# Optimization experiments

Hardware: AMD Instinct MI355X
Metric: run time of the kernel (lower is better)

## Reference

```python
import jax, jax.numpy as jnp
import numpy as np

DIM = 1024
HEADS = 8
HD = DIM // HEADS          # 128
HALF = HD // 2             # 64 complex pairs
EPS = 1e-6
T, L, H, W = 10, 4, 21, 37
TOK_PER_FRAME = 1 + L * (5 + H * W)   # 3129
SK = T * TOK_PER_FRAME                # 31290
SQ = 512
THETA = 10000.0


def _inv_freqs(dim):
    # matches precompute_freqs_cis: 1/theta**(arange(0,dim,2)/dim)
    return 1.0 / THETA ** (np.arange(0, dim, 2)[: dim // 2].astype(np.float64) / dim)


def _angles(t_idx, h_idx, w_idx):
    # 3D RoPE split per precompute_freqs_cis_3d: f gets HD-2*(HD//3)=44 dims, h/w get HD//3=42 each
    hd3 = HD // 3
    inv_f = _inv_freqs(HD - 2 * hd3)  # 22 freqs
    inv_h = _inv_freqs(hd3)           # 21 freqs
    inv_w = _inv_freqs(hd3)           # 21 freqs
    ang = np.concatenate([
        t_idx[:, None] * inv_f[None, :],
        h_idx[:, None] * inv_h[None, :],
        w_idx[:, None] * inv_w[None, :],
    ], axis=-1)  # [S, 64]
    return ang


def _memory_positions():
    # per-frame layout from build_3d_freqs_unified: 1 pose token (h=w=0),
    # then per layer: 5 register tokens (h=w=0) + H*W grid tokens
    h_f, w_f = [0], [0]
    grid_h, grid_w = np.meshgrid(np.arange(H), np.arange(W), indexing='ij')
    for _ in range(L):
        h_f += [0] * 5 + list(grid_h.ravel())
        w_f += [0] * 5 + list(grid_w.ravel())
    h_f = np.asarray(h_f, np.float64)
    w_f = np.asarray(w_f, np.float64)
    t_idx = np.repeat(np.arange(T, dtype=np.float64), TOK_PER_FRAME)
    return t_idx, np.tile(h_f, T), np.tile(w_f, T)


def setup_inputs() -> dict:
    key = jax.random.key(0)
    ks = jax.random.split(key, 8)
    # RoPE angle tables
    tq = np.zeros(SQ)  # use_time_encoding=False for queries -> t=0
    hq = (np.arange(SQ) // W) % H
    wq = np.arange(SQ) % W
    ang_q = _angles(tq.astype(np.float64), hq.astype(np.float64), wq.astype(np.float64))
    tk, hk, wk = _memory_positions()
    ang_k = _angles(tk, hk, wk)
    s = 0.02
    inp = {
        'x': jax.random.normal(ks[0], (1, SQ, DIM), jnp.float32),
        'mem': jax.random.normal(ks[1], (1, SK, DIM), jnp.float32),
        'mask': jax.random.randint(ks[2], (1, SK), 0, 2) > 0,
        'cos_q': jnp.asarray(np.cos(ang_q), jnp.float32),
        'sin_q': jnp.asarray(np.sin(ang_q), jnp.float32),
        'cos_k': jnp.asarray(np.cos(ang_k), jnp.float32),
        'sin_k': jnp.asarray(np.sin(ang_k), jnp.float32),
        'Wq': jax.random.normal(ks[3], (DIM, DIM), jnp.float32) * s,
        'bq': jnp.zeros((DIM,), jnp.float32),
        'Wk': jax.random.normal(ks[4], (DIM, DIM), jnp.float32) * s,
        'bk': jnp.zeros((DIM,), jnp.float32),
        'Wv': jax.random.normal(ks[5], (DIM, DIM), jnp.float32) * s,
        'bv': jnp.zeros((DIM,), jnp.float32),
        'Wo': jax.random.normal(ks[6], (DIM, DIM), jnp.float32) * s,
        'bo': jnp.zeros((DIM,), jnp.float32),
        'gq': jnp.ones((DIM,), jnp.float32),
        'gk': jnp.ones((DIM,), jnp.float32),
    }
    return inp


def _rmsnorm(x, g):
    xf = x.astype(jnp.float32)
    y = xf * jax.lax.rsqrt(jnp.mean(xf * xf, axis=-1, keepdims=True) + EPS)
    return y.astype(x.dtype) * g


def _rope(x, cos, sin):
    # x: [B,S,D]; complex rotation on interleaved pairs per head, freqs shared across heads
    B, S, _ = x.shape
    xh = x.reshape(B, S, HEADS, HALF, 2)
    xr, xi = xh[..., 0], xh[..., 1]
    c = cos[None, :, None, :]
    s = sin[None, :, None, :]
    orr = xr * c - xi * s
    oi = xr * s + xi * c
    return jnp.stack([orr, oi], axis=-1).reshape(B, S, HEADS * HD)


def reference(x, mem, mask, cos_q, sin_q, cos_k, sin_k,
              Wq, bq, Wk, bk, Wv, bv, Wo, bo, gq, gk):
    q = _rmsnorm(x @ Wq.T + bq, gq)
    k = _rmsnorm(mem @ Wk.T + bk, gk)
    v = mem @ Wv.T + bv
    q = _rope(q, cos_q, sin_q)
    k = _rope(k, cos_k, sin_k)
    B, Sq, _ = q.shape
    Sk = k.shape[1]
    qh = q.reshape(B, Sq, HEADS, HD)
    kh = k.reshape(B, Sk, HEADS, HD)
    vh = v.reshape(B, Sk, HEADS, HD)
    scores = jnp.einsum('bqnd,bknd->bnqk', qh, kh) / jnp.sqrt(jnp.float32(HD))
    bias = jnp.where(mask[:, None, None, :], 0.0, -jnp.inf).astype(scores.dtype)
    attn = jax.nn.softmax(scores + bias, axis=-1)
    out = jnp.einsum('bnqk,bknd->bqnd', attn, vh).reshape(B, Sq, DIM)
    return out @ Wo.T + bo
```

## Files before the change

kernel.cpp:

```cpp
#include <hip/hip_runtime.h>
#include <cstdint>

typedef __bf16 bf16;
typedef __bf16 bf16x8 __attribute__((ext_vector_type(8)));
typedef __bf16 bf16x4 __attribute__((ext_vector_type(4)));
typedef float f32x4 __attribute__((ext_vector_type(4)));

#define DEVINL __device__ __forceinline__

namespace {
constexpr int DIM = 1024, HEADS = 8, HD = 128, HALF = 64;
constexpr int SQ = 512;
constexpr int SK = 31290;
constexpr int SKP = 31488;
constexpr int NSPLIT = 24;

constexpr long OFF_MEMB = 0;
constexpr long OFF_XB   = OFF_MEMB + (long)SKP * DIM * 2;
constexpr long OFF_WKV  = OFF_XB + (long)SQ * DIM * 2;
constexpr long OFF_WQ   = OFF_WKV + 2048L * DIM * 2;
constexpr long OFF_WO   = OFF_WQ + (long)DIM * DIM * 2;
constexpr long OFF_BKV  = OFF_WO + (long)DIM * DIM * 2;
constexpr long OFF_KPRE = OFF_BKV + 2048L * 4;
constexpr long OFF_VT   = OFF_KPRE + (long)SKP * DIM * 2;
constexpr long OFF_QPRE = OFF_VT + (long)DIM * SKP * 2;
constexpr long OFF_QR   = OFF_QPRE + (long)SQ * DIM * 4;
constexpr long OFF_ML   = OFF_QR + (long)SQ * DIM * 2;
constexpr long OFF_AO   = OFF_ML + (long)NSPLIT * HEADS * SQ * 2 * 4;
constexpr long OFF_IDX  = OFF_AO + (long)SQ * DIM * 2;
constexpr long OFF_NKC  = OFF_IDX + 31744L * 4;
constexpr long OFF_OP   = OFF_MEMB;
}

DEVINL void gl_lds16(const void* g, void* l) {
  __builtin_amdgcn_global_load_lds(
      (__attribute__((address_space(1))) void*)(void*)g,
      (__attribute__((address_space(3))) void*)l, 16, 0, 0);
}


__global__ __launch_bounds__(1024) void k_scan(const int* __restrict__ mask,
                                               int* __restrict__ idx,
                                               int* __restrict__ nkcp) {
  int tid = threadIdx.x, lane = tid & 63, wv = tid >> 6;
  __shared__ int wsum[16];
  __shared__ int base;
  if (tid == 0) base = 0;
  __syncthreads();
  for (int c = 0; c < 31; ++c) {
    int i = c * 1024 + tid;
    int m = (i < SK) ? (mask[i] != 0) : 0;
    unsigned long long bal = __ballot(m);
    int wpre = (int)__popcll(bal & ((1ull << lane) - 1ull));
    if (lane == 0) wsum[wv] = (int)__popcll(bal);
    __syncthreads();
    int woff = 0;
    #pragma unroll
    for (int j = 0; j < 16; ++j) woff += (j < wv) ? wsum[j] : 0;
    if (m) idx[base + woff + wpre] = i;
    __syncthreads();
    if (tid == 0) {
      int tot = 0;
      #pragma unroll
      for (int j = 0; j < 16; ++j) tot += wsum[j];
      base += tot;
    }
    __syncthreads();
  }
  if (tid == 0) *nkcp = base;
}


__global__ __launch_bounds__(256) void k_cvt_mem(const float* __restrict__ mem,
                                                 const int* __restrict__ idx,
                                                 const int* __restrict__ nkcp,
                                                 bf16* __restrict__ memb) {
  long i = (long)blockIdx.x * 256 + threadIdx.x;
  long e = i * 8;
  if (e >= (long)SKP * DIM) return;
  int row = (int)(e >> 10);
  int nkc = *nkcp;
  int lim = ((((nkc + 63) & ~63) + 255) & ~255);
  if (row >= lim) return;
  bf16x8 o;
  if (row < nkc) {
    long se = ((long)idx[row] << 10) + (e & 1023);
    float4 a = *(const float4*)(mem + se);
    float4 b = *(const float4*)(mem + se + 4);
    o[0] = (bf16)a.x; o[1] = (bf16)a.y; o[2] = (bf16)a.z; o[3] = (bf16)a.w;
    o[4] = (bf16)b.x; o[5] = (bf16)b.y; o[6] = (bf16)b.z; o[7] = (bf16)b.w;
  } else {
    #pragma unroll
    for (int j = 0; j < 8; ++j) o[j] = (bf16)0.0f;
  }
  *(bf16x8*)(memb + e) = o;
}

__global__ __launch_bounds__(256) void k_prep(const float* __restrict__ x,
    const float* __restrict__ Wq, const float* __restrict__ Wo,
    const float* __restrict__ Wk, const float* __restrict__ Wv,
    const float* __restrict__ bk, const float* __restrict__ bv,
    bf16* __restrict__ xb, bf16* __restrict__ WqB, bf16* __restrict__ WoB,
    bf16* __restrict__ WkvB, float* __restrict__ bKV) {
  long i = (long)blockIdx.x * 256 + threadIdx.x;
  constexpr long n_x = 65536, n_w = 131072;
  const float* src;
  bf16* dst;
  long off;
  if (i < n_x) { src = x; dst = xb; off = i; }
  else if (i < n_x + n_w) { src = Wq; dst = WqB; off = i - n_x; }
  else if (i < n_x + 2 * n_w) { src = Wo; dst = WoB; off = i - n_x - n_w; }
  else if (i < n_x + 2 * n_w + 262144) {
    long j = i - n_x - 2 * n_w;
    long e = j * 8;
    int n = (int)(e >> 10);
    const float* s2 = (n < 1024) ? (Wk + e) : (Wv + e - 1024L * 1024);
    float4 a = *(const float4*)(s2);
    float4 b = *(const float4*)(s2 + 4);
    bf16x8 o;
    o[0] = (bf16)a.x; o[1] = (bf16)a.y; o[2] = (bf16)a.z; o[3] = (bf16)a.w;
    o[4] = (bf16)b.x; o[5] = (bf16)b.y; o[6] = (bf16)b.z; o[7] = (bf16)b.w;
    *(bf16x8*)(WkvB + e) = o;
    if (j < 2048) bKV[j] = (j < 1024) ? bk[j] : bv[j - 1024];
    return;
  } else return;
  long e = off * 8;
  float4 a = *(const float4*)(src + e);
  float4 b = *(const float4*)(src + e + 4);
  bf16x8 o;
  o[0] = (bf16)a.x; o[1] = (bf16)a.y; o[2] = (bf16)a.z; o[3] = (bf16)a.w;
  o[4] = (bf16)b.x; o[5] = (bf16)b.y; o[6] = (bf16)b.z; o[7] = (bf16)b.w;
  *(bf16x8*)(dst + e) = o;
}


template<int MODE>
__global__ __launch_bounds__(256, 2)
void k_gemm(const bf16* __restrict__ A, const bf16* __restrict__ B,
            const float* __restrict__ bias, int Mtiles, int Ntiles,
            float* __restrict__ outF, int ldF,
            bf16* __restrict__ outK, bf16* __restrict__ outVT) {
  constexpr int K = 1024;
  __shared__ char lds[32768];
  char* ldsA = lds;
  char* ldsB = lds + 16384;
  int tid = threadIdx.x;
  int w = tid >> 6, lane = tid & 63;
  int cpx = gridDim.x >> 3;
  int bid = (blockIdx.x & 7) * cpx + (blockIdx.x >> 3);
  int mt = bid / Ntiles, nt = bid % Ntiles;
  int m0 = mt * 128, n0 = nt * 128;
  int wm = w >> 1, wn = w & 1;
  int cl = lane & 15, rg = lane >> 4;

  f32x4 acc[4][4] = {};

  int rowi = lane >> 3, g = lane & 7;
  for (int kt = 0; kt < K / 64; ++kt) {
    #pragma unroll
    for (int j = 0; j < 4; ++j) {
      int rb = (w * 4 + j) * 8;
      int row = rb + rowi;
      int gs = g ^ (row & 7);
      gl_lds16((const char*)(A + (long)(m0 + row) * K + kt * 64) + gs * 16, ldsA + rb * 128);
      gl_lds16((const char*)(B + (long)(n0 + row) * K + kt * 64) + gs * 16, ldsB + rb * 128);
    }
    __syncthreads();
    #pragma unroll
    for (int ks = 0; ks < 2; ++ks) {
      bf16x8 af[4], bfr[4];
      #pragma unroll
      for (int i = 0; i < 4; ++i) {
        int rowA = wm * 64 + i * 16 + cl;
        int c = ks * 4 + rg;
        af[i] = *(const bf16x8*)(ldsA + rowA * 128 + ((c ^ (rowA & 7)) * 16));
        int rowB = wn * 64 + i * 16 + cl;
        bfr[i] = *(const bf16x8*)(ldsB + rowB * 128 + ((c ^ (rowB & 7)) * 16));
      }
      #pragma unroll
      for (int mf = 0; mf < 4; ++mf)
        #pragma unroll
        for (int nf = 0; nf < 4; ++nf)
          acc[mf][nf] = __builtin_amdgcn_mfma_f32_16x16x32_bf16(af[mf], bfr[nf], acc[mf][nf], 0, 0, 0);
    }
    __syncthreads();
  }

  #pragma unroll
  for (int mf = 0; mf < 4; ++mf) {
    #pragma unroll
    for (int nf = 0; nf < 4; ++nf) {
      int n = n0 + wn * 64 + nf * 16 + cl;
      float bval = bias[n];
      int mb = m0 + wm * 64 + mf * 16 + rg * 4;
      #pragma unroll
      for (int rr = 0; rr < 4; ++rr)
        outF[(long)(mb + rr) * ldF + n] = acc[mf][nf][rr] + bval;
    }
  }
}


#define KV_PHASE(P)                                                                   \
  {                                                                                   \
    bf16x8 a00 = dsA(cur, 2 * (P), 0),     a01 = dsA(cur, 2 * (P), 1);                \
    bf16x8 a10 = dsA(cur, 2 * (P) + 1, 0), a11 = dsA(cur, 2 * (P) + 1, 1);            \
    __builtin_amdgcn_s_setprio(1);                                                    \
    _Pragma("unroll")                                                                 \
    for (int nf = 0; nf < 4; ++nf) {                                                  \
      acc[2 * (P)][nf]     = __builtin_amdgcn_mfma_f32_16x16x32_bf16(a00, bb[nf][0], acc[2 * (P)][nf], 0, 0, 0);     \
      acc[2 * (P) + 1][nf] = __builtin_amdgcn_mfma_f32_16x16x32_bf16(a10, bb[nf][0], acc[2 * (P) + 1][nf], 0, 0, 0); \
    }                                                                                 \
    _Pragma("unroll")                                                                 \
    for (int nf = 0; nf < 4; ++nf) {                                                  \
      acc[2 * (P)][nf]     = __builtin_amdgcn_mfma_f32_16x16x32_bf16(a01, bb[nf][1], acc[2 * (P)][nf], 0, 0, 0);     \
      acc[2 * (P) + 1][nf] = __builtin_amdgcn_mfma_f32_16x16x32_bf16(a11, bb[nf][1], acc[2 * (P) + 1][nf], 0, 0, 0); \
    }                                                                                 \
    __builtin_amdgcn_s_setprio(0);                                                    \
  }

__global__ __launch_bounds__(512)
void k_gemm_kv(const bf16* __restrict__ A, const bf16* __restrict__ B,
               const float* __restrict__ bias, const int* __restrict__ nkcp,
               bf16* __restrict__ outK, bf16* __restrict__ outVT) {
  constexpr int K = 1024, NTK = 16;
  __shared__ char lds[131072];
  const int tid = threadIdx.x;
  const int w = tid >> 6, lane = tid & 63;
  const int mt = blockIdx.x >> 3, nt = blockIdx.x & 7;
  const int m0 = mt * 256, n0 = nt * 256;
  if (m0 >= ((*nkcp + 63) & ~63)) return;
  const int wm = w >> 2, wn = w & 3;
  const int cl = lane & 15, rg = lane >> 4;
  const int srow = lane >> 3, sg = lane & 7;

  f32x4 acc[8][4] = {};

  auto stage = [&](int b, int kt, int isB, int cr) {
    const bf16* src = isB ? B : A;
    int r = cr + w * 8 + srow;
    int gs = sg ^ (r & 7);
    const char* gp = (const char*)(src + (long)((isB ? n0 : m0) + r) * K + kt * 64) + gs * 16;
    char* lp = lds + b * 65536 + isB * 32768 + (cr + w * 8) * 128;
    gl_lds16(gp, lp);
  };
  auto dsA = [&](int b, int mf, int ks) -> bf16x8 {
    int r = wm * 128 + mf * 16 + cl;
    int c = ks * 4 + rg;
    return *(const bf16x8*)(lds + b * 65536 + r * 128 + ((c ^ (r & 7)) * 16));
  };
  auto dsB = [&](int b, int nf, int ks) -> bf16x8 {
    int r = wn * 64 + nf * 16 + cl;
    int c = ks * 4 + rg;
    return *(const bf16x8*)(lds + b * 65536 + 32768 + r * 128 + ((c ^ (r & 7)) * 16));
  };

  stage(0, 0, 1, 0);   stage(0, 0, 1, 64);
  stage(0, 0, 1, 128); stage(0, 0, 1, 192);
  stage(0, 0, 0, 0);   stage(0, 0, 0, 128);
  stage(0, 0, 0, 64);  stage(0, 0, 0, 192);

  for (int t = 0; t < NTK; ++t) {
    const int cur = t & 1, nxt = cur ^ 1;
    const bool pre = (t + 1 < NTK);
    bf16x8 bb[4][2];

    if (pre) {
      stage(nxt, t + 1, 1, 0); stage(nxt, t + 1, 1, 64);
      asm volatile("s_waitcnt vmcnt(4)\ns_barrier" ::: "memory");
    } else {
      asm volatile("s_waitcnt vmcnt(2)\ns_barrier" ::: "memory");
    }
    #pragma unroll
    for (int nf = 0; nf < 4; ++nf) { bb[nf][0] = dsB(cur, nf, 0); bb[nf][1] = dsB(cur, nf, 1); }
    KV_PHASE(0)
    asm volatile("s_barrier" ::: "memory");
    if (pre) { stage(nxt, t + 1, 1, 128); stage(nxt, t + 1, 1, 192); }
    KV_PHASE(1)
    asm volatile("s_barrier" ::: "memory");
    if (pre) {
      stage(nxt, t + 1, 0, 0); stage(nxt, t + 1, 0, 128);
      asm volatile("s_waitcnt vmcnt(6)\ns_barrier" ::: "memory");
    } else {
      asm volatile("s_waitcnt vmcnt(0)\ns_barrier" ::: "memory");
    }
    KV_PHASE(2)
    asm volatile("s_barrier" ::: "memory");
    if (pre) { stage(nxt, t + 1, 0, 64); stage(nxt, t + 1, 0, 192); }
    KV_PHASE(3)
    asm volatile("s_barrier" ::: "memory");
  }

  if (nt < 4) {
    #pragma unroll
    for (int mf = 0; mf < 8; ++mf)
      #pragma unroll
      for (int nf = 0; nf < 4; ++nf) {
        int n = n0 + wn * 64 + nf * 16 + cl;
        float bval = bias[n];
        int mrow = m0 + wm * 128 + mf * 16 + rg * 4;
        #pragma unroll
        for (int rr = 0; rr < 4; ++rr)
          outK[(long)(mrow + rr) * 1024 + n] = (bf16)(acc[mf][nf][rr] + bval);
      }
  } else {
    #pragma unroll
    for (int mf = 0; mf < 8; ++mf)
      #pragma unroll
      for (int nf = 0; nf < 4; ++nf) {
        int n = n0 + wn * 64 + nf * 16 + cl;
        float bval = bias[n];
        int mrow = m0 + wm * 128 + mf * 16 + rg * 4;
        bf16x4 pk;
        #pragma unroll
        for (int rr = 0; rr < 4; ++rr) pk[rr] = (bf16)(acc[mf][nf][rr] + bval);
        *(bf16x4*)(outVT + (long)(n - 1024) * SKP + mrow) = pk;
      }
  }
}


__global__ __launch_bounds__(256) void k_fuse_q(const float* __restrict__ QP,
    bf16* __restrict__ Qr, const float* __restrict__ gg,
    const float* __restrict__ cosT, const float* __restrict__ sinT) {
  int row = blockIdx.x, tid = threadIdx.x;
  int d0 = tid * 4;
  float4 t = *(const float4*)(QP + (long)row * DIM + d0);
  float v0 = t.x, v1 = t.y, v2 = t.z, v3 = t.w;
  float ss = v0 * v0 + v1 * v1 + v2 * v2 + v3 * v3;
  #pragma unroll
  for (int m = 1; m < 64; m <<= 1) ss += __shfl_xor(ss, m);
  __shared__ float red[4];
  if ((tid & 63) == 0) red[tid >> 6] = ss;
  __syncthreads();
  float rn = rsqrtf((red[0] + red[1] + red[2] + red[3]) * (1.0f / DIM) + 1e-6f);
  v0 *= rn * gg[d0]; v1 *= rn * gg[d0 + 1]; v2 *= rn * gg[d0 + 2]; v3 *= rn * gg[d0 + 3];
  int i0 = (d0 & 127) >> 1;
  float c0 = cosT[(long)row * HALF + i0], s0 = sinT[(long)row * HALF + i0];
  float c1 = cosT[(long)row * HALF + i0 + 1], s1 = sinT[(long)row * HALF + i0 + 1];
  bf16x4 o = { (bf16)(v0 * c0 - v1 * s0), (bf16)(v0 * s0 + v1 * c0),
               (bf16)(v2 * c1 - v3 * s1), (bf16)(v2 * s1 + v3 * c1) };
  *(bf16x4*)(Qr + (long)row * DIM + d0) = o;
}

__global__ __launch_bounds__(256) void k_fuse_k(bf16* __restrict__ KP,
    const float* __restrict__ gg, const float* __restrict__ cosT,
    const float* __restrict__ sinT, const int* __restrict__ idx,
    const int* __restrict__ nkcp) {
  int row = blockIdx.x, tid = threadIdx.x;
  int nkc = *nkcp;
  if (row >= ((nkc + 63) & ~63)) return;
  int orig = (row < nkc) ? idx[row] : 0;
  int d0 = tid * 4;
  bf16x4 t = *(const bf16x4*)(KP + (long)row * DIM + d0);
  float v0 = (float)t[0], v1 = (float)t[1], v2 = (float)t[2], v3 = (float)t[3];
  float ss = v0 * v0 + v1 * v1 + v2 * v2 + v3 * v3;
  #pragma unroll
  for (int m = 1; m < 64; m <<= 1) ss += __shfl_xor(ss, m);
  __shared__ float red[4];
  if ((tid & 63) == 0) red[tid >> 6] = ss;
  __syncthreads();
  float rn = rsqrtf((red[0] + red[1] + red[2] + red[3]) * (1.0f / DIM) + 1e-6f);
  v0 *= rn * gg[d0]; v1 *= rn * gg[d0 + 1]; v2 *= rn * gg[d0 + 2]; v3 *= rn * gg[d0 + 3];
  int i0 = (d0 & 127) >> 1;
  float c0 = cosT[(long)orig * HALF + i0], s0 = sinT[(long)orig * HALF + i0];
  float c1 = cosT[(long)orig * HALF + i0 + 1], s1 = sinT[(long)orig * HALF + i0 + 1];
  bf16x4 o = { (bf16)(v0 * c0 - v1 * s0), (bf16)(v0 * s0 + v1 * c0),
               (bf16)(v2 * c1 - v3 * s1), (bf16)(v2 * s1 + v3 * c1) };
  *(bf16x4*)(KP + (long)row * DIM + d0) = o;
}


__global__ __launch_bounds__(256, 2)
void k_attn(const bf16* __restrict__ Kr, const bf16* __restrict__ VT,
            const bf16* __restrict__ Qr, const int* __restrict__ nkcp,
            float* __restrict__ Opart, float* __restrict__ ml) {
  __shared__ char lds[51200];
  char* ldsK = lds;
  char* ldsV = lds + 16384;
  int tid = threadIdx.x, w = tid >> 6, lane = tid & 63;
  char* ldsP = lds + 32768 + w * 4608;
  int bid = blockIdx.x;
  int swz = (bid & 7) * 96 + (bid >> 3);
  int sp = swz >> 5, h = (swz >> 2) & 7, qb = swz & 3;
  int nkc = *nkcp;
  int NTC = (nkc + 63) >> 6;
  int t0 = (sp * NTC) / NSPLIT;
  int t1 = ((sp + 1) * NTC) / NSPLIT;
  int cl = lane & 15, rg = lane >> 4;
  int qbase = qb * 128 + w * 32;

  bf16x8 qf[2][4];
  #pragma unroll
  for (int mf = 0; mf < 2; ++mf)
    #pragma unroll
    for (int ks = 0; ks < 4; ++ks)
      qf[mf][ks] = *(const bf16x8*)(Qr + (long)(qbase + mf * 16 + cl) * DIM + h * HD + ks * 32 + rg * 8);

  f32x4 Oa[2][8] = {};
  float m_r[2] = {-1e30f, -1e30f};
  float l_r[2] = {0.f, 0.f};

  const float sc = 0.08838834764831845f;
  for (int t = t0; t < t1; ++t) {
    int k0 = t * 64;
    __syncthreads();
    {
      int rK = lane >> 4, gK = lane & 15;
      #pragma unroll
      for (int j = 0; j < 4; ++j) {
        int rb = w * 16 + j * 4;
        int row = rb + rK;
        int gs = gK ^ (row & 7);
        gl_lds16((const char*)(Kr + (long)(k0 + row) * DIM + h * HD) + gs * 16,
                 ldsK + rb * 256);
      }
      int rV = lane >> 3, gV = lane & 7;
      #pragma unroll
      for (int j = 0; j < 4; ++j) {
        int db = w * 32 + j * 8;
        int d = db + rV;
        int gs = gV ^ (d & 7);
        gl_lds16((const char*)(VT + (long)(h * HD + d) * SKP + k0) + gs * 16,
                 ldsV + db * 128);
      }
    }
    __syncthreads();

    f32x4 sa[2][4] = {};
    #pragma unroll
    for (int ks = 0; ks < 4; ++ks) {
      #pragma unroll
      for (int nf = 0; nf < 4; ++nf) {
        int key = nf * 16 + cl;
        int c = ks * 4 + rg;
        bf16x8 kb = *(const bf16x8*)(ldsK + key * 256 + ((c ^ (key & 7)) * 16));
        sa[0][nf] = __builtin_amdgcn_mfma_f32_16x16x32_bf16(kb, qf[0][ks], sa[0][nf], 0, 0, 0);
        sa[1][nf] = __builtin_amdgcn_mfma_f32_16x16x32_bf16(kb, qf[1][ks], sa[1][nf], 0, 0, 0);
      }
    }

    #pragma unroll
    for (int mf = 0; mf < 2; ++mf) {
      #pragma unroll
      for (int nf = 0; nf < 4; ++nf)
        #pragma unroll
        for (int r = 0; r < 4; ++r) {
          int key = k0 + nf * 16 + rg * 4 + r;
          sa[mf][nf][r] = (key < nkc) ? sa[mf][nf][r] * sc : -1e30f;
        }
      float mx = sa[mf][0][0];
      #pragma unroll
      for (int nf = 0; nf < 4; ++nf)
        #pragma unroll
        for (int r = 0; r < 4; ++r) mx = fmaxf(mx, sa[mf][nf][r]);
      mx = fmaxf(mx, __shfl_xor(mx, 16));
      mx = fmaxf(mx, __shfl_xor(mx, 32));
      bool grew = mx > m_r[mf] + 6.0f;
      if (__any(grew)) {
        float mn = grew ? mx : m_r[mf];
        float scl = __expf(m_r[mf] - mn);
        m_r[mf] = mn;
        l_r[mf] *= scl;
        int sb = lane & 48;
        float s0 = __shfl(scl, sb | (rg * 4 + 0));
        float s1 = __shfl(scl, sb | (rg * 4 + 1));
        float s2 = __shfl(scl, sb | (rg * 4 + 2));
        float s3 = __shfl(scl, sb | (rg * 4 + 3));
        #pragma unroll
        for (int df = 0; df < 8; ++df) {
          Oa[mf][df][0] *= s0; Oa[mf][df][1] *= s1;
          Oa[mf][df][2] *= s2; Oa[mf][df][3] *= s3;
        }
      }
      float rsum = 0.f;
      #pragma unroll
      for (int nf = 0; nf < 4; ++nf)
        #pragma unroll
        for (int r = 0; r < 4; ++r) {
          float p = __expf(sa[mf][nf][r] - m_r[mf]);
          sa[mf][nf][r] = p;
          rsum += p;
        }
      rsum += __shfl_xor(rsum, 16);
      rsum += __shfl_xor(rsum, 32);
      l_r[mf] += rsum;
      char* prow = ldsP + (mf * 16 + cl) * 144;
      #pragma unroll
      for (int nf = 0; nf < 4; ++nf) {
        bf16x4 pk = { (bf16)sa[mf][nf][0], (bf16)sa[mf][nf][1],
                      (bf16)sa[mf][nf][2], (bf16)sa[mf][nf][3] };
        *(bf16x4*)(prow + nf * 32 + rg * 8) = pk;
      }
    }

    #pragma unroll
    for (int ks = 0; ks < 2; ++ks) {
      bf16x8 pa0 = *(const bf16x8*)(ldsP + cl * 144 + ks * 64 + rg * 16);
      bf16x8 pa1 = *(const bf16x8*)(ldsP + (16 + cl) * 144 + ks * 64 + rg * 16);
      int c = ks * 4 + rg;
      #pragma unroll
      for (int df = 0; df < 8; ++df) {
        int d = df * 16 + cl;
        bf16x8 vb = *(const bf16x8*)(ldsV + d * 128 + ((c ^ (d & 7)) * 16));
        Oa[0][df] = __builtin_amdgcn_mfma_f32_16x16x32_bf16(pa0, vb, Oa[0][df], 0, 0, 0);
        Oa[1][df] = __builtin_amdgcn_mfma_f32_16x16x32_bf16(pa1, vb, Oa[1][df], 0, 0, 0);
      }
    }
  }

  long rowb = (long)(sp * HEADS + h) * SQ + qbase;
  #pragma unroll
  for (int mf = 0; mf < 2; ++mf) {
    #pragma unroll
    for (int df = 0; df < 8; ++df)
      #pragma unroll
      for (int r = 0; r < 4; ++r) {
        int qr = mf * 16 + rg * 4 + r;
        Opart[(rowb + qr) * HD + df * 16 + cl] = Oa[mf][df][r];
      }
  }
  if (rg == 0) {
    #pragma unroll
    for (int mf = 0; mf < 2; ++mf) {
      ml[(rowb + mf * 16 + cl) * 2] = m_r[mf];
      ml[(rowb + mf * 16 + cl) * 2 + 1] = l_r[mf];
    }
  }
}

__global__ __launch_bounds__(128) void k_combine(const float* __restrict__ Opart,
    const float* __restrict__ ml, bf16* __restrict__ AO) {
  int bid = blockIdx.x;
  int h = bid >> 9, qq = bid & 511;
  int d = threadIdx.x;
  float M = -1e30f;
  #pragma unroll 4
  for (int s2 = 0; s2 < NSPLIT; ++s2) {
    long mi = (long)(s2 * HEADS + h) * SQ + qq;
    M = fmaxf(M, ml[mi * 2]);
  }
  float L = 0.f, acc = 0.f;
  #pragma unroll 4
  for (int s2 = 0; s2 < NSPLIT; ++s2) {
    long mi = (long)(s2 * HEADS + h) * SQ + qq;
    float wgt = __expf(ml[mi * 2] - M);
    L += wgt * ml[mi * 2 + 1];
    acc += wgt * Opart[mi * HD + d];
  }
  AO[(long)qq * DIM + h * HD + d] = (bf16)(acc / L);
}


extern "C" void kernel_launch(void* const* d_in, const int* in_sizes, int n_in,
                              void* d_out, int out_size, void* d_ws, size_t ws_size,
                              hipStream_t stream) {
  const float* x     = (const float*)d_in[0];
  const float* mem   = (const float*)d_in[1];
  const int*   mask  = (const int*)d_in[2];
  const float* cos_q = (const float*)d_in[3];
  const float* sin_q = (const float*)d_in[4];
  const float* cos_k = (const float*)d_in[5];
  const float* sin_k = (const float*)d_in[6];
  const float* Wq    = (const float*)d_in[7];
  const float* bq    = (const float*)d_in[8];
  const float* Wk    = (const float*)d_in[9];
  const float* bk    = (const float*)d_in[10];
  const float* Wv    = (const float*)d_in[11];
  const float* bv    = (const float*)d_in[12];
  const float* Wo    = (const float*)d_in[13];
  const float* bo    = (const float*)d_in[14];
  const float* gq    = (const float*)d_in[15];
  const float* gk    = (const float*)d_in[16];

  char* ws = (char*)d_ws;
  bf16*  memb = (bf16*)(ws + OFF_MEMB);
  bf16*  xb   = (bf16*)(ws + OFF_XB);
  bf16*  WkvB = (bf16*)(ws + OFF_WKV);
  bf16*  WqB  = (bf16*)(ws + OFF_WQ);
  bf16*  WoB  = (bf16*)(ws + OFF_WO);
  float* bKV  = (float*)(ws + OFF_BKV);
  bf16*  Kpre = (bf16*)(ws + OFF_KPRE);
  bf16*  VT   = (bf16*)(ws + OFF_VT);
  float* Qpre = (float*)(ws + OFF_QPRE);
  bf16*  Qr   = (bf16*)(ws + OFF_QR);
  float* Opart= (float*)(ws + OFF_OP);
  float* mlb  = (float*)(ws + OFF_ML);
  bf16*  AO   = (bf16*)(ws + OFF_AO);
  int*   idx  = (int*)(ws + OFF_IDX);
  int*   nkcp = (int*)(ws + OFF_NKC);

  k_scan<<<dim3(1), dim3(1024), 0, stream>>>(mask, idx, nkcp);
  k_cvt_mem<<<dim3(SKP * DIM / 8 / 256), dim3(256), 0, stream>>>(mem, idx, nkcp, memb);
  k_prep<<<dim3(2304), dim3(256), 0, stream>>>(x, Wq, Wo, Wk, Wv, bk, bv,
                                               xb, WqB, WoB, WkvB, bKV);

  k_gemm<0><<<dim3(4 * 8), dim3(256), 0, stream>>>(xb, WqB, bq, 4, 8, Qpre, DIM,
                                                   (bf16*)nullptr, (bf16*)nullptr);
  k_gemm_kv<<<dim3(984), dim3(512), 0, stream>>>(memb, WkvB, bKV, nkcp, Kpre, VT);

  k_fuse_q<<<dim3(SQ), dim3(256), 0, stream>>>(Qpre, Qr, gq, cos_q, sin_q);
  k_fuse_k<<<dim3(SKP), dim3(256), 0, stream>>>(Kpre, gk, cos_k, sin_k, idx, nkcp);

  k_attn<<<dim3(NSPLIT * HEADS * 4), dim3(256), 0, stream>>>(Kpre, VT, Qr, nkcp, Opart, mlb);
  k_combine<<<dim3(HEADS * SQ), dim3(128), 0, stream>>>(Opart, mlb, AO);

  k_gemm<0><<<dim3(4 * 8), dim3(256), 0, stream>>>(AO, WoB, bo, 4, 8, (float*)d_out, DIM,
                                                   (bf16*)nullptr, (bf16*)nullptr);
  (void)in_sizes; (void)n_in; (void)out_size; (void)ws_size;
}
```

Measured before the change: 255.4 us.

## Parallelize mask compaction scan across blocks and reshuffle KV GEMM prefetch staging

Replaces the single-block serial 31-iteration mask compaction with a three-kernel multi-block scan: per-chunk counts, a wave-level prefix over the chunk counts, then a parallel scatter of indices. This is meant to remove the serial latency of one workgroup looping with barriers, at the cost of two extra kernel launches. Separately, the KV GEMM loop now issues next-tile loads earlier, in phases 1 and 2 instead of 1-3, with the waitcnt adjusted. The aim is to give the loads more time to overlap with MFMA work.

```diff
diff --git a/kernel.cpp b/kernel.cpp
--- a/kernel.cpp
+++ b/kernel.cpp
@@ -14,6 +14,7 @@
 constexpr int SK = 31290;
 constexpr int SKP = 31488;
 constexpr int NSPLIT = 24;
+constexpr int NCHUNK = 31;
 
 constexpr long OFF_MEMB = 0;
 constexpr long OFF_XB   = OFF_MEMB + (long)SKP * DIM * 2;
@@ -29,6 +30,8 @@
 constexpr long OFF_AO   = OFF_ML + (long)NSPLIT * HEADS * SQ * 2 * 4;
 constexpr long OFF_IDX  = OFF_AO + (long)SQ * DIM * 2;
 constexpr long OFF_NKC  = OFF_IDX + 31744L * 4;
+constexpr long OFF_CSM  = OFF_NKC + 64;
+constexpr long OFF_CBS  = OFF_CSM + 256;
 constexpr long OFF_OP   = OFF_MEMB;
 }
 
@@ -39,35 +42,53 @@
 }
 
 
-__global__ __launch_bounds__(1024) void k_scan(const int* __restrict__ mask,
-                                               int* __restrict__ idx,
-                                               int* __restrict__ nkcp) {
+__global__ __launch_bounds__(1024) void k_scan1(const int* __restrict__ mask,
+                                                int* __restrict__ csum) {
   int tid = threadIdx.x, lane = tid & 63, wv = tid >> 6;
   __shared__ int wsum[16];
-  __shared__ int base;
-  if (tid == 0) base = 0;
+  long i = (long)blockIdx.x * 1024 + tid;
+  int m = (i < SK) ? (mask[i] != 0) : 0;
+  unsigned long long bal = __ballot(m);
+  if (lane == 0) wsum[wv] = (int)__popcll(bal);
   __syncthreads();
-  for (int c = 0; c < 31; ++c) {
-    int i = c * 1024 + tid;
-    int m = (i < SK) ? (mask[i] != 0) : 0;
-    unsigned long long bal = __ballot(m);
-    int wpre = (int)__popcll(bal & ((1ull << lane) - 1ull));
-    if (lane == 0) wsum[wv] = (int)__popcll(bal);
-    __syncthreads();
-    int woff = 0;
-    #pragma unroll
-    for (int j = 0; j < 16; ++j) woff += (j < wv) ? wsum[j] : 0;
-    if (m) idx[base + woff + wpre] = i;
-    __syncthreads();
-    if (tid == 0) {
-      int tot = 0;
-      #pragma unroll
-      for (int j = 0; j < 16; ++j) tot += wsum[j];
-      base += tot;
-    }
-    __syncthreads();
-  }
-  if (tid == 0) *nkcp = base;
+  if (tid == 0) {
+    int tot = 0;
+    #pragma unroll
+    for (int j = 0; j < 16; ++j) tot += wsum[j];
+    csum[blockIdx.x] = tot;
+  }
+}
+
+__global__ __launch_bounds__(64) void k_scan2(const int* __restrict__ csum,
+                                              int* __restrict__ cbase,
+                                              int* __restrict__ nkcp) {
+  int lane = threadIdx.x;
+  int v = (lane < NCHUNK) ? csum[lane] : 0;
+  int p = v;
+  #pragma unroll
+  for (int off = 1; off < 64; off <<= 1) {
+    int t = __shfl_up(p, off);
+    if (lane >= off) p += t;
+  }
+  if (lane < NCHUNK) cbase[lane] = p - v;
+  if (lane == NCHUNK - 1) *nkcp = p;
+}
+
+__global__ __launch_bounds__(1024) void k_scan3(const int* __restrict__ mask,
+                                                const int* __restrict__ cbase,
+                                                int* __restrict__ idx) {
+  int tid = threadIdx.x, lane = tid & 63, wv = tid >> 6;
+  __shared__ int wsum[16];
+  long i = (long)blockIdx.x * 1024 + tid;
+  int m = (i < SK) ? (mask[i] != 0) : 0;
+  unsigned long long bal = __ballot(m);
+  int wpre = (int)__popcll(bal & ((1ull << lane) - 1ull));
+  if (lane == 0) wsum[wv] = (int)__popcll(bal);
+  __syncthreads();
+  int woff = 0;
+  #pragma unroll
+  for (int j = 0; j < 16; ++j) woff += (j < wv) ? wsum[j] : 0;
+  if (m) idx[cbase[blockIdx.x] + woff + wpre] = (int)i;
 }
 
 
@@ -275,18 +296,20 @@
     for (int nf = 0; nf < 4; ++nf) { bb[nf][0] = dsB(cur, nf, 0); bb[nf][1] = dsB(cur, nf, 1); }
     KV_PHASE(0)
     asm volatile("s_barrier" ::: "memory");
-    if (pre) { stage(nxt, t + 1, 1, 128); stage(nxt, t + 1, 1, 192); }
+    if (pre) {
+      stage(nxt, t + 1, 1, 128); stage(nxt, t + 1, 1, 192);
+      stage(nxt, t + 1, 0, 0);   stage(nxt, t + 1, 0, 128);
+    }
     KV_PHASE(1)
     asm volatile("s_barrier" ::: "memory");
     if (pre) {
-      stage(nxt, t + 1, 0, 0); stage(nxt, t + 1, 0, 128);
-      asm volatile("s_waitcnt vmcnt(6)\ns_barrier" ::: "memory");
+      stage(nxt, t + 1, 0, 64); stage(nxt, t + 1, 0, 192);
+      asm volatile("s_waitcnt vmcnt(8)\ns_barrier" ::: "memory");
     } else {
       asm volatile("s_waitcnt vmcnt(0)\ns_barrier" ::: "memory");
     }
     KV_PHASE(2)
     asm volatile("s_barrier" ::: "memory");
-    if (pre) { stage(nxt, t + 1, 0, 64); stage(nxt, t + 1, 0, 192); }
     KV_PHASE(3)
     asm volatile("s_barrier" ::: "memory");
   }
@@ -589,8 +612,12 @@
   bf16*  AO   = (bf16*)(ws + OFF_AO);
   int*   idx  = (int*)(ws + OFF_IDX);
   int*   nkcp = (int*)(ws + OFF_NKC);
-
-  k_scan<<<dim3(1), dim3(1024), 0, stream>>>(mask, idx, nkcp);
+  int*   csum = (int*)(ws + OFF_CSM);
+  int*   cbase= (int*)(ws + OFF_CBS);
+
+  k_scan1<<<dim3(NCHUNK), dim3(1024), 0, stream>>>(mask, csum);
+  k_scan2<<<dim3(1), dim3(64), 0, stream>>>(csum, cbase, nkcp);
+  k_scan3<<<dim3(NCHUNK), dim3(1024), 0, stream>>>(mask, cbase, idx);
   k_cvt_mem<<<dim3(SKP * DIM / 8 / 256), dim3(256), 0, stream>>>(mem, idx, nkcp, memb);
   k_prep<<<dim3(2304), dim3(256), 0, stream>>>(x, Wq, Wo, Wk, Wv, bk, bv,
                                                xb, WqB, WoB, WkvB, bKV);
```

Result: faster. 236.7 us, median of 3 (-7.3%).
